# Optimization experiments

Hardware: AMD Instinct MI355X
Metric: run time of the kernel (lower is better)

Reference implementation:

```python
import jax, jax.numpy as jnp
import numpy as np

B, T, C = 2, 2048, 1024
H = 16
HD = C // H  # head_size = 64
FF = 2 * C   # ffwd_size default = n_embd * 2
EPS = float(jnp.finfo(jnp.float32).eps)  # torch RMSNorm eps=None -> finfo eps


def rmsnorm(x, g):
    # torch.nn.RMSNorm: x / sqrt(mean(x^2) + eps) * weight
    ms = jnp.mean(jnp.square(x), axis=-1, keepdims=True)
    return x * jax.lax.rsqrt(ms + EPS) * g


def setup_inputs() -> dict:
    key = jax.random.key(0)
    ks = jax.random.split(key, 12)
    s_in = 1.0 / np.sqrt(C)
    s_ff = 1.0 / np.sqrt(FF)
    return {
        "target": jax.random.normal(ks[0], (B, T, C), dtype=jnp.float32),
        # per-head projections, torch Linear layout [out, in] stacked over heads: [H, HD, C]
        "wq": jax.random.uniform(ks[1], (H, HD, C), jnp.float32, -s_in, s_in),
        "wk": jax.random.uniform(ks[2], (H, HD, C), jnp.float32, -s_in, s_in),
        "wv": jax.random.uniform(ks[3], (H, HD, C), jnp.float32, -s_in, s_in),
        "w_proj": jax.random.uniform(ks[4], (C, H * HD), jnp.float32, -s_in, s_in),
        "b_proj": jax.random.uniform(ks[5], (C,), jnp.float32, -s_in, s_in),
        "w1": jax.random.uniform(ks[6], (FF, C), jnp.float32, -s_in, s_in),
        "b1": jax.random.uniform(ks[7], (FF,), jnp.float32, -s_in, s_in),
        "w2": jax.random.uniform(ks[8], (C, FF), jnp.float32, -s_ff, s_ff),
        "b2": jax.random.uniform(ks[9], (C,), jnp.float32, -s_ff, s_ff),
        "g1": jnp.ones((C,), jnp.float32),
        "g2": jnp.ones((C,), jnp.float32),
    }


def reference(target, wq, wk, wv, w_proj, b_proj, w1, b1, w2, b2, g1, g2):
    x = rmsnorm(target, g1)
    # q,k,v: [B,H,T,HD]
    q = jnp.einsum("btc,hdc->bhtd", x, wq)
    k = jnp.einsum("btc,hdc->bhtd", x, wk)
    v = jnp.einsum("btc,hdc->bhtd", x, wv)
    scale = HD ** -0.5
    wei = jnp.einsum("bhtd,bhsd->bhts", q, k) * scale  # [B,H,T,T]
    causal = jnp.tril(jnp.ones((T, T), dtype=bool))
    wei = jnp.where(causal, wei, -jnp.inf)
    wei = jax.nn.softmax(wei, axis=-1)
    attn = jnp.einsum("bhts,bhsd->bhtd", wei, v)  # [B,H,T,HD]
    attn = attn.transpose(0, 2, 1, 3).reshape(B, T, H * HD)  # concat heads
    attn = attn @ w_proj.T + b_proj
    target = target + attn
    y = rmsnorm(target, g2)
    h = jax.nn.gelu(y @ w1.T + b1, approximate=False)  # torch nn.GELU default = exact
    ff = h @ w2.T + b2
    return target + ff
```

## Files before the change

kernel.cpp:

```cpp
#include <hip/hip_runtime.h>
#include <math.h>

#define B_  2
#define T_  2048
#define C_  1024
#define H_  16
#define HD_ 64
#define FF_ 2048
#define EPS_ 1.1920929e-07f

typedef __attribute__((ext_vector_type(8))) short short8;
typedef __attribute__((ext_vector_type(4))) float f32x4;

__device__ __forceinline__ unsigned short f2bf(float f) {
    unsigned u = __float_as_uint(f);
    u += 0x7fffu + ((u >> 16) & 1u);
    return (unsigned short)(u >> 16);
}
__device__ __forceinline__ float bf2f(unsigned short u) {
    return __uint_as_float(((unsigned)u) << 16);
}

__global__ void prep_kernel(const float* __restrict__ wq, const float* __restrict__ wk,
                            const float* __restrict__ wv, const float* __restrict__ wp,
                            const float* __restrict__ w1, const float* __restrict__ w2,
                            unsigned short* __restrict__ wb,
                            const float* __restrict__ x, const float* __restrict__ g,
                            unsigned short* __restrict__ y) {
    int tid = threadIdx.x;
    if (blockIdx.x < 8192) {
        size_t i = ((size_t)blockIdx.x * 256 + tid) * 4;
        const float* src; size_t off = i;
        if      (i < 1048576u)  { src = wq; }
        else if (i < 2097152u)  { src = wk; off = i - 1048576u; }
        else if (i < 3145728u)  { src = wv; off = i - 2097152u; }
        else if (i < 4194304u)  { src = wp; off = i - 3145728u; }
        else if (i < 6291456u)  { src = w1; off = i - 4194304u; }
        else                    { src = w2; off = i - 6291456u; }
        float4 v4 = *(const float4*)(src + off);
        ushort4 o4;
        o4.x = f2bf(v4.x); o4.y = f2bf(v4.y); o4.z = f2bf(v4.z); o4.w = f2bf(v4.w);
        *(ushort4*)(wb + i) = o4;
    } else {
        int row = blockIdx.x - 8192;
        const float4* xr = (const float4*)(x + (size_t)row * C_);
        float4 xv = xr[tid];
        float ss = xv.x * xv.x + xv.y * xv.y + xv.z * xv.z + xv.w * xv.w;
        #pragma unroll
        for (int m = 32; m >= 1; m >>= 1) ss += __shfl_xor(ss, m, 64);
        __shared__ float sred[4];
        if ((tid & 63) == 0) sred[tid >> 6] = ss;
        __syncthreads();
        float tot = sred[0] + sred[1] + sred[2] + sred[3];
        float r = rsqrtf(tot * (1.0f / C_) + EPS_);
        float4 gv = ((const float4*)g)[tid];
        ushort4 o;
        o.x = f2bf(xv.x * r * gv.x);
        o.y = f2bf(xv.y * r * gv.y);
        o.z = f2bf(xv.z * r * gv.z);
        o.w = f2bf(xv.w * r * gv.w);
        *((ushort4*)(y + (size_t)row * C_) + tid) = o;
    }
}

__global__ void rmsnorm_bf16_kernel(const float* __restrict__ x, const float* __restrict__ g,
                                    unsigned short* __restrict__ y) {
    int row = blockIdx.x;
    int tid = threadIdx.x;
    const float4* xr = (const float4*)(x + (size_t)row * C_);
    float4 xv = xr[tid];
    float ss = xv.x * xv.x + xv.y * xv.y + xv.z * xv.z + xv.w * xv.w;
    #pragma unroll
    for (int m = 32; m >= 1; m >>= 1) ss += __shfl_xor(ss, m, 64);
    __shared__ float sred[4];
    if ((tid & 63) == 0) sred[tid >> 6] = ss;
    __syncthreads();
    float tot = sred[0] + sred[1] + sred[2] + sred[3];
    float r = rsqrtf(tot * (1.0f / C_) + EPS_);
    float4 gv = ((const float4*)g)[tid];
    ushort4 o;
    o.x = f2bf(xv.x * r * gv.x);
    o.y = f2bf(xv.y * r * gv.y);
    o.z = f2bf(xv.z * r * gv.z);
    o.w = f2bf(xv.w * r * gv.w);
    *((ushort4*)(y + (size_t)row * C_) + tid) = o;
}

template <int TM, int ACT, bool BIAS, bool RES, bool OBF16, int ROUTE>
__global__ __launch_bounds__(256) void mfma_gemm(
        const unsigned short* __restrict__ A, const unsigned short* __restrict__ W,
        const float* __restrict__ bias, const float* __restrict__ resid,
        void* __restrict__ O0, void* __restrict__ O1, void* __restrict__ O2,
        int M, int N, int K) {
    constexpr int ACH = TM / 8;
    constexpr int NCH = (ACH + 16) / 4;
    constexpr int MI  = TM / 32;
    __shared__ short As[2 * TM * 32];
    __shared__ short Bs[2 * 128 * 32];
    const int tid  = threadIdx.x;
    const int w    = tid >> 6, lane = tid & 63;
    const int tileN = blockIdx.x * 128, tileM = blockIdx.y * TM;

    const unsigned short* gsrc[NCH];
    short* ldst[NCH];
    #pragma unroll
    for (int i2 = 0; i2 < NCH; ++i2) {
        int c = w * NCH + i2;
        if (c < ACH) {
            int kh = c / (ACH / 2), lc = c % (ACH / 2);
            gsrc[i2] = A + (size_t)(tileM + lc * 16 + (lane >> 2)) * K + kh * 32 + (lane & 3) * 8;
            ldst[i2] = As + c * 512;
        } else {
            int c2 = c - ACH;
            int kh = c2 >> 3, lc = c2 & 7;
            gsrc[i2] = W + (size_t)(tileN + lc * 16 + (lane >> 2)) * K + kh * 32 + (lane & 3) * 8;
            ldst[i2] = Bs + c2 * 512;
        }
    }

    f32x4 acc[MI][4];
    const f32x4 zed = {0.f, 0.f, 0.f, 0.f};
    #pragma unroll
    for (int i = 0; i < MI; ++i)
        #pragma unroll
        for (int j = 0; j < 4; ++j) acc[i][j] = zed;

    const int wm = (w >> 1) * (TM / 2), wn = (w & 1) * 64;
    const int frow = lane & 15, koff = (lane >> 4) * 8;

    for (int k0 = 0; k0 < K; k0 += 64) {
        #pragma unroll
        for (int i2 = 0; i2 < NCH; ++i2)
            __builtin_amdgcn_global_load_lds(
                (const __attribute__((address_space(1))) unsigned*)(gsrc[i2] + k0),
                (__attribute__((address_space(3))) unsigned*)ldst[i2], 16, 0, 0);
        __syncthreads();

        #pragma unroll
        for (int kh = 0; kh < 2; ++kh) {
            short8 af[MI], bfr[4];
            #pragma unroll
            for (int i = 0; i < MI; ++i)
                af[i] = *(const short8*)(As + kh * TM * 32 + (wm + i * 16 + frow) * 32 + koff);
            #pragma unroll
            for (int j = 0; j < 4; ++j)
                bfr[j] = *(const short8*)(Bs + kh * 128 * 32 + (wn + j * 16 + frow) * 32 + koff);
            #pragma unroll
            for (int i = 0; i < MI; ++i)
                #pragma unroll
                for (int j = 0; j < 4; ++j)
                    acc[i][j] = __builtin_amdgcn_mfma_f32_16x16x32_bf16(af[i], bfr[j], acc[i][j], 0, 0, 0);
        }
        __syncthreads();
    }

    const int ecol = lane & 15, erow = (lane >> 4) * 4;
    const int zone = ROUTE ? (tileN >> 10) : 0;
    #pragma unroll
    for (int j = 0; j < 4; ++j) {
        int n = tileN + wn + j * 16 + ecol;
        float bv = BIAS ? bias[n] : 0.f;
        int nl = ROUTE ? (n & 1023) : n;
        #pragma unroll
        for (int i = 0; i < MI; ++i) {
            int mbase = tileM + wm + i * 16 + erow;
            #pragma unroll
            for (int r = 0; r < 4; ++r) {
                float val = acc[i][j][r] + bv;
                if (ACT == 1) val = 0.5f * val * (1.0f + erff(val * 0.70710678118654752f));
                int mrow = mbase + r;
                if (ROUTE) {
                    if (zone == 0) {
                        ((unsigned short*)O0)[(size_t)mrow * 1024 + nl] = f2bf(val * 0.125f);
                    } else if (zone == 1) {
                        ((unsigned short*)O1)[(size_t)mrow * 1024 + nl] = f2bf(val);
                    } else {
                        int bb = mrow >> 11, tt = mrow & 2047;
                        int hh = nl >> 6, dd = nl & 63;
                        ((unsigned short*)O2)[((size_t)((bb * 16 + hh) * 64 + dd)) * 2048 + tt] = f2bf(val);
                    }
                } else {
                    size_t idx = (size_t)mrow * N + n;
                    if (RES) val += resid[idx];
                    if (OBF16) ((unsigned short*)O0)[idx] = f2bf(val);
                    else       ((float*)O0)[idx] = val;
                }
            }
        }
    }
}

__global__ __launch_bounds__(256) void flash_mfma_kernel(
        const unsigned short* __restrict__ q, const unsigned short* __restrict__ k,
        const unsigned short* __restrict__ vT, unsigned short* __restrict__ out) {
    __shared__ unsigned short Ks[64 * 68];
    __shared__ unsigned short Vt[80 * 68];
    __shared__ unsigned short Ps[4 * 16 * 68];

    const int tid  = threadIdx.x;
    const int w    = tid >> 6, lane = tid & 63;
    const int quad = lane >> 4, l15 = lane & 15;
    const int bh = blockIdx.x;
    const int qt = (gridDim.y - 1) - blockIdx.y;
    const int h = bh & (H_ - 1);
    const int b = bh >> 4;

    const size_t qkbase = (size_t)b * T_ * C_ + h * HD_;
    const size_t vbase  = (size_t)(b * H_ + h) * HD_ * T_;

    for (int idx = tid; idx < 16 * 68; idx += 256) {
        int rr = idx / 68;
        Vt[(64 + rr) * 68 + (idx % 68)] = (rr == 0) ? (unsigned short)0x3F80 : (unsigned short)0;
    }

    short8 QB[2];
    {
        const unsigned short* qp = q + qkbase + (size_t)(qt * 64 + w * 16 + l15) * C_;
        QB[0] = *(const short8*)(qp + quad * 8);
        QB[1] = *(const short8*)(qp + 32 + quad * 8);
    }

    f32x4 O[4], O5;
    const f32x4 zed = {0.f, 0.f, 0.f, 0.f};
    #pragma unroll
    for (int dt = 0; dt < 4; ++dt) O[dt] = zed;
    O5 = zed;

    const int qg = qt * 64 + w * 16 + l15;
    const int psoff = w * 1088 + l15 * 68;
    const int sr = tid >> 3, sp = tid & 7;

    for (int st = 0; st <= qt; ++st) {
        const int s0 = st * 64;
        {
            const unsigned short* kp = k + qkbase + (size_t)(s0 + sr) * C_ + sp * 8;
            *(short8*)&Ks[sr * 68 + sp * 8]        = *(const short8*)kp;
            *(short8*)&Ks[(sr + 32) * 68 + sp * 8] = *(const short8*)(kp + 32 * C_);
            const unsigned short* vp = vT + vbase + (size_t)sr * T_ + s0 + sp * 8;
            *(short8*)&Vt[sr * 68 + sp * 8]        = *(const short8*)vp;
            *(short8*)&Vt[(sr + 32) * 68 + sp * 8] = *(const short8*)(vp + 32 * T_);
        }
        __syncthreads();

        f32x4 S[4];
        #pragma unroll
        for (int u = 0; u < 4; ++u) {
            const unsigned short* kr = &Ks[(16 * u + l15) * 68 + quad * 8];
            short8 KA0 = *(const short8*)kr;
            short8 KA1 = *(const short8*)(kr + 32);
            S[u] = __builtin_amdgcn_mfma_f32_16x16x32_bf16(KA0, QB[0], zed, 0, 0, 0);
            S[u] = __builtin_amdgcn_mfma_f32_16x16x32_bf16(KA1, QB[1], S[u], 0, 0, 0);
        }

        float pv[16];
        if (st == qt) {
            #pragma unroll
            for (int u = 0; u < 4; ++u)
                #pragma unroll
                for (int r = 0; r < 4; ++r) {
                    int sg = s0 + 16 * u + quad * 4 + r;
                    pv[u * 4 + r] = (sg > qg) ? 0.f : __expf(S[u][r]);
                }
        } else {
            #pragma unroll
            for (int u = 0; u < 4; ++u)
                #pragma unroll
                for (int r = 0; r < 4; ++r)
                    pv[u * 4 + r] = __expf(S[u][r]);
        }

        #pragma unroll
        for (int u = 0; u < 4; ++u) {
            uint2 pw;
            pw.x = (unsigned)f2bf(pv[u * 4 + 0]) | ((unsigned)f2bf(pv[u * 4 + 1]) << 16);
            pw.y = (unsigned)f2bf(pv[u * 4 + 2]) | ((unsigned)f2bf(pv[u * 4 + 3]) << 16);
            *(uint2*)&Ps[psoff + 16 * u + quad * 4] = pw;
        }
        __syncthreads();

        #pragma unroll
        for (int kh = 0; kh < 2; ++kh) {
            short8 PA = *(const short8*)&Ps[psoff + kh * 32 + quad * 8];
            #pragma unroll
            for (int dt = 0; dt < 4; ++dt) {
                short8 VB = *(const short8*)&Vt[(16 * dt + l15) * 68 + kh * 32 + quad * 8];
                O[dt] = __builtin_amdgcn_mfma_f32_16x16x32_bf16(PA, VB, O[dt], 0, 0, 0);
            }
            short8 VB5 = *(const short8*)&Vt[(64 + l15) * 68 + kh * 32 + quad * 8];
            O5 = __builtin_amdgcn_mfma_f32_16x16x32_bf16(PA, VB5, O5, 0, 0, 0);
        }
        __syncthreads();
    }

    f32x4 inv;
    #pragma unroll
    for (int r = 0; r < 4; ++r) inv[r] = 1.0f / __shfl(O5[r], quad * 16, 64);
    #pragma unroll
    for (int dt = 0; dt < 4; ++dt)
        #pragma unroll
        for (int r = 0; r < 4; ++r) {
            int row = qt * 64 + w * 16 + quad * 4 + r;
            int col = h * HD_ + dt * 16 + l15;
            out[((size_t)(b * T_ + row)) * C_ + col] = f2bf(O[dt][r] * inv[r]);
        }
}

extern "C" void kernel_launch(void* const* d_in, const int* in_sizes, int n_in,
                              void* d_out, int out_size, void* d_ws, size_t ws_size,
                              hipStream_t stream) {
    const float* target = (const float*)d_in[0];
    const float* wq     = (const float*)d_in[1];
    const float* wk     = (const float*)d_in[2];
    const float* wv     = (const float*)d_in[3];
    const float* w_proj = (const float*)d_in[4];
    const float* b_proj = (const float*)d_in[5];
    const float* w1     = (const float*)d_in[6];
    const float* b1     = (const float*)d_in[7];
    const float* w2     = (const float*)d_in[8];
    const float* b2     = (const float*)d_in[9];
    const float* g1     = (const float*)d_in[10];
    const float* g2     = (const float*)d_in[11];
    float* out = (float*)d_out;

    char* ws = (char*)d_ws;
    const size_t MB = 1u << 20;
    unsigned short* xn = (unsigned short*)(ws);
    unsigned short* q  = (unsigned short*)(ws + 8 * MB);
    unsigned short* k  = (unsigned short*)(ws + 16 * MB);
    unsigned short* vt = (unsigned short*)(ws + 24 * MB);
    float*          x2 = (float*)(ws + 32 * MB);
    unsigned short* wb = (unsigned short*)(ws + 48 * MB);
    unsigned short* y  = q;
    unsigned short* hb = k;

    unsigned short* wqkv_b = wb;
    unsigned short* wp_b   = wb + 3145728u;
    unsigned short* w1_b   = wb + 4194304u;
    unsigned short* w2_b   = wb + 6291456u;

    const int M = B_ * T_;

    prep_kernel<<<12288, 256, 0, stream>>>(wq, wk, wv, w_proj, w1, w2, wb, target, g1, xn);

    mfma_gemm<128, 0, false, false, true, 1><<<dim3(24, M / 128), 256, 0, stream>>>(
        xn, wqkv_b, nullptr, nullptr, q, k, vt, M, 3072, C_);

    flash_mfma_kernel<<<dim3(B_ * H_, T_ / 64), 256, 0, stream>>>(q, k, vt, xn);

    mfma_gemm<64, 0, true, true, false, 0><<<dim3(C_ / 128, M / 64), 256, 0, stream>>>(
        xn, wp_b, b_proj, target, x2, nullptr, nullptr, M, C_, C_);

    rmsnorm_bf16_kernel<<<M, 256, 0, stream>>>(x2, g2, y);

    mfma_gemm<64, 1, true, false, true, 0><<<dim3(FF_ / 128, M / 64), 256, 0, stream>>>(
        y, w1_b, b1, nullptr, hb, nullptr, nullptr, M, FF_, C_);

    mfma_gemm<64, 0, true, true, false, 0><<<dim3(C_ / 128, M / 64), 256, 0, stream>>>(
        hb, w2_b, b2, x2, out, nullptr, nullptr, M, C_, FF_);
}
```

Measured before the change: 342.1 us.

## Compute softmax row sums with shuffles instead of extra ones-column MFMA

The flash attention kernel no longer appends a ones-row to the V tile to get the softmax denominator through an extra MFMA. It now sums the exponentials in registers and reduces them with cross-lane shuffles. The S tile is handled in two 32-wide halves with double-buffered P staging, and the LDS row pitch changes from 68 to 72. This drops one MFMA and its LDS reads per half-tile and shrinks shared memory, but adds a barrier per half and computes the sum from fp32 values rather than the bf16-rounded P.

```diff
diff --git a/kernel.cpp b/kernel.cpp
--- a/kernel.cpp
+++ b/kernel.cpp
@@ -193,9 +193,9 @@
 __global__ __launch_bounds__(256) void flash_mfma_kernel(
         const unsigned short* __restrict__ q, const unsigned short* __restrict__ k,
         const unsigned short* __restrict__ vT, unsigned short* __restrict__ out) {
-    __shared__ unsigned short Ks[64 * 68];
-    __shared__ unsigned short Vt[80 * 68];
-    __shared__ unsigned short Ps[4 * 16 * 68];
+    __shared__ unsigned short Ks[64 * 72];
+    __shared__ unsigned short Vt[64 * 72];
+    __shared__ unsigned short Ps[2 * 4 * 16 * 40];
 
     const int tid  = threadIdx.x;
     const int w    = tid >> 6, lane = tid & 63;
@@ -208,11 +208,6 @@
     const size_t qkbase = (size_t)b * T_ * C_ + h * HD_;
     const size_t vbase  = (size_t)(b * H_ + h) * HD_ * T_;
 
-    for (int idx = tid; idx < 16 * 68; idx += 256) {
-        int rr = idx / 68;
-        Vt[(64 + rr) * 68 + (idx % 68)] = (rr == 0) ? (unsigned short)0x3F80 : (unsigned short)0;
-    }
-
     short8 QB[2];
     {
         const unsigned short* qp = q + qkbase + (size_t)(qt * 64 + w * 16 + l15) * C_;
@@ -220,81 +215,86 @@
         QB[1] = *(const short8*)(qp + 32 + quad * 8);
     }
 
-    f32x4 O[4], O5;
+    f32x4 O[4];
     const f32x4 zed = {0.f, 0.f, 0.f, 0.f};
     #pragma unroll
     for (int dt = 0; dt < 4; ++dt) O[dt] = zed;
-    O5 = zed;
+    float l_i = 0.f;
 
     const int qg = qt * 64 + w * 16 + l15;
-    const int psoff = w * 1088 + l15 * 68;
+    const int psoff = w * 640 + l15 * 40;
     const int sr = tid >> 3, sp = tid & 7;
 
     for (int st = 0; st <= qt; ++st) {
         const int s0 = st * 64;
         {
             const unsigned short* kp = k + qkbase + (size_t)(s0 + sr) * C_ + sp * 8;
-            *(short8*)&Ks[sr * 68 + sp * 8]        = *(const short8*)kp;
-            *(short8*)&Ks[(sr + 32) * 68 + sp * 8] = *(const short8*)(kp + 32 * C_);
+            *(short8*)&Ks[sr * 72 + sp * 8]        = *(const short8*)kp;
+            *(short8*)&Ks[(sr + 32) * 72 + sp * 8] = *(const short8*)(kp + 32 * C_);
             const unsigned short* vp = vT + vbase + (size_t)sr * T_ + s0 + sp * 8;
-            *(short8*)&Vt[sr * 68 + sp * 8]        = *(const short8*)vp;
-            *(short8*)&Vt[(sr + 32) * 68 + sp * 8] = *(const short8*)(vp + 32 * T_);
-        }
-        __syncthreads();
-
-        f32x4 S[4];
-        #pragma unroll
-        for (int u = 0; u < 4; ++u) {
-            const unsigned short* kr = &Ks[(16 * u + l15) * 68 + quad * 8];
-            short8 KA0 = *(const short8*)kr;
-            short8 KA1 = *(const short8*)(kr + 32);
-            S[u] = __builtin_amdgcn_mfma_f32_16x16x32_bf16(KA0, QB[0], zed, 0, 0, 0);
-            S[u] = __builtin_amdgcn_mfma_f32_16x16x32_bf16(KA1, QB[1], S[u], 0, 0, 0);
-        }
-
-        float pv[16];
-        if (st == qt) {
-            #pragma unroll
-            for (int u = 0; u < 4; ++u)
+            *(short8*)&Vt[sr * 72 + sp * 8]        = *(const short8*)vp;
+            *(short8*)&Vt[(sr + 32) * 72 + sp * 8] = *(const short8*)(vp + 32 * T_);
+        }
+        __syncthreads();
+
+        const bool diag = (st == qt);
+        #pragma unroll
+        for (int sb = 0; sb < 2; ++sb) {
+            const int sbl = sb * 32;
+            f32x4 Sacc[2];
+            #pragma unroll
+            for (int u = 0; u < 2; ++u) {
+                const unsigned short* kr = &Ks[(sbl + 16 * u + l15) * 72 + quad * 8];
+                short8 KA0 = *(const short8*)kr;
+                short8 KA1 = *(const short8*)(kr + 32);
+                Sacc[u] = __builtin_amdgcn_mfma_f32_16x16x32_bf16(KA0, QB[0], zed, 0, 0, 0);
+                Sacc[u] = __builtin_amdgcn_mfma_f32_16x16x32_bf16(KA1, QB[1], Sacc[u], 0, 0, 0);
+            }
+            float vals[8];
+            if (diag) {
                 #pragma unroll
-                for (int r = 0; r < 4; ++r) {
-                    int sg = s0 + 16 * u + quad * 4 + r;
-                    pv[u * 4 + r] = (sg > qg) ? 0.f : __expf(S[u][r]);
-                }
-        } else {
-            #pragma unroll
-            for (int u = 0; u < 4; ++u)
+                for (int u = 0; u < 2; ++u)
+                    #pragma unroll
+                    for (int r = 0; r < 4; ++r) {
+                        int sg = s0 + sbl + 16 * u + quad * 4 + r;
+                        vals[u * 4 + r] = (sg > qg) ? 0.f : __expf(Sacc[u][r]);
+                    }
+            } else {
                 #pragma unroll
-                for (int r = 0; r < 4; ++r)
-                    pv[u * 4 + r] = __expf(S[u][r]);
-        }
-
-        #pragma unroll
-        for (int u = 0; u < 4; ++u) {
-            uint2 pw;
-            pw.x = (unsigned)f2bf(pv[u * 4 + 0]) | ((unsigned)f2bf(pv[u * 4 + 1]) << 16);
-            pw.y = (unsigned)f2bf(pv[u * 4 + 2]) | ((unsigned)f2bf(pv[u * 4 + 3]) << 16);
-            *(uint2*)&Ps[psoff + 16 * u + quad * 4] = pw;
-        }
-        __syncthreads();
-
-        #pragma unroll
-        for (int kh = 0; kh < 2; ++kh) {
-            short8 PA = *(const short8*)&Ps[psoff + kh * 32 + quad * 8];
+                for (int u = 0; u < 2; ++u)
+                    #pragma unroll
+                    for (int r = 0; r < 4; ++r)
+                        vals[u * 4 + r] = __expf(Sacc[u][r]);
+            }
+            float rs = 0.f;
+            #pragma unroll
+            for (int i = 0; i < 8; ++i) rs += vals[i];
+            rs += __shfl_xor(rs, 16, 64);
+            rs += __shfl_xor(rs, 32, 64);
+            l_i += rs;
+
+            #pragma unroll
+            for (int u = 0; u < 2; ++u) {
+                uint2 pw;
+                pw.x = (unsigned)f2bf(vals[u * 4 + 0]) | ((unsigned)f2bf(vals[u * 4 + 1]) << 16);
+                pw.y = (unsigned)f2bf(vals[u * 4 + 2]) | ((unsigned)f2bf(vals[u * 4 + 3]) << 16);
+                *(uint2*)&Ps[sb * 2560 + psoff + 16 * u + quad * 4] = pw;
+            }
+            __syncthreads();
+
+            short8 PA = *(const short8*)&Ps[sb * 2560 + psoff + quad * 8];
             #pragma unroll
             for (int dt = 0; dt < 4; ++dt) {
-                short8 VB = *(const short8*)&Vt[(16 * dt + l15) * 68 + kh * 32 + quad * 8];
+                short8 VB = *(const short8*)&Vt[(16 * dt + l15) * 72 + sbl + quad * 8];
                 O[dt] = __builtin_amdgcn_mfma_f32_16x16x32_bf16(PA, VB, O[dt], 0, 0, 0);
             }
-            short8 VB5 = *(const short8*)&Vt[(64 + l15) * 68 + kh * 32 + quad * 8];
-            O5 = __builtin_amdgcn_mfma_f32_16x16x32_bf16(PA, VB5, O5, 0, 0, 0);
         }
         __syncthreads();
     }
 
     f32x4 inv;
     #pragma unroll
-    for (int r = 0; r < 4; ++r) inv[r] = 1.0f / __shfl(O5[r], quad * 16, 64);
+    for (int r = 0; r < 4; ++r) inv[r] = 1.0f / __shfl(l_i, quad * 4 + r, 64);
     #pragma unroll
     for (int dt = 0; dt < 4; ++dt)
         #pragma unroll
```

Result: faster. 292.7 us (-14.5%).
